# Optimization experiments

Measured on AMD Instinct MI355X. Metric: run time of the kernel, lower is better.

Reference implementation:

```python
import jax, jax.numpy as jnp
import numpy as np

N_ATOMS = 100000
M_NBR = 12
ORIG_FEA = 92
NBR_FEA = 41
AF = 64          # atom_fea_len
N_CONV = 3
OUT_DIM = 128
N_CRYSTALS = 2000
ATOMS_PER = 50
EPS = 1e-5


def setup_inputs() -> dict:
    key = jax.random.key(0)
    ks = jax.random.split(key, 12)
    inp = {
        "atom_fea": jax.random.normal(ks[0], (N_ATOMS, ORIG_FEA), dtype=jnp.float32),
        "nbr_fea": jax.random.normal(ks[1], (N_ATOMS, M_NBR, NBR_FEA), dtype=jnp.float32),
        "nbr_fea_idx": jax.random.randint(ks[2], (N_ATOMS, M_NBR), 0, N_ATOMS, dtype=jnp.int32),
        "crystal_atom_idx": jnp.arange(N_CRYSTALS * ATOMS_PER, dtype=jnp.int32).reshape(N_CRYSTALS, ATOMS_PER),
    }
    # parameters
    inp["W_embed"] = jax.random.normal(ks[3], (ORIG_FEA, AF), dtype=jnp.float32) * 0.05
    inp["b_embed"] = jnp.zeros((AF,), dtype=jnp.float32)
    in_full = 2 * AF + NBR_FEA  # 169
    inp["W_full"] = jax.random.normal(ks[4], (N_CONV, in_full, 2 * AF), dtype=jnp.float32) * 0.05
    inp["b_full"] = jnp.zeros((N_CONV, 2 * AF), dtype=jnp.float32)
    inp["bn1_gamma"] = jnp.ones((N_CONV, 2 * AF), dtype=jnp.float32)
    inp["bn1_beta"] = jnp.zeros((N_CONV, 2 * AF), dtype=jnp.float32)
    inp["bn2_gamma"] = jnp.ones((N_CONV, AF), dtype=jnp.float32)
    inp["bn2_beta"] = jnp.zeros((N_CONV, AF), dtype=jnp.float32)
    inp["W_pool"] = jax.random.normal(ks[5], (AF, OUT_DIM), dtype=jnp.float32) * 0.05
    inp["b_pool"] = jnp.zeros((OUT_DIM,), dtype=jnp.float32)
    return inp


def _batchnorm(x, gamma, beta):
    # training-mode BatchNorm1d over leading dim, biased variance
    m = jnp.mean(x, axis=0)
    v = jnp.var(x, axis=0)
    return (x - m) * jax.lax.rsqrt(v + EPS) * gamma + beta


def _conv_layer(x, nbr_fea, nbr_fea_idx, Wf, bf, g1, be1, g2, be2):
    N, M = nbr_fea_idx.shape
    nbr_atom = x[nbr_fea_idx]                                  # [N, M, AF] gather
    self_fea = jnp.broadcast_to(x[:, None, :], (N, M, AF))     # [N, M, AF]
    total = jnp.concatenate([self_fea, nbr_atom, nbr_fea], axis=2)  # [N, M, 2AF+NBR]
    gated = jnp.einsum('nmi,io->nmo', total, Wf) + bf          # [N, M, 2AF]
    gated = _batchnorm(gated.reshape(N * M, 2 * AF), g1, be1).reshape(N, M, 2 * AF)
    nbr_filter = jax.nn.sigmoid(gated[..., :AF])
    nbr_core = jax.nn.softplus(gated[..., AF:])
    nbr_sumed = jnp.sum(nbr_filter * nbr_core, axis=1)         # [N, AF]
    nbr_sumed = _batchnorm(nbr_sumed, g2, be2)
    return jax.nn.softplus(x + nbr_sumed)


def reference(atom_fea, nbr_fea, nbr_fea_idx, crystal_atom_idx,
              W_embed, b_embed, W_full, b_full,
              bn1_gamma, bn1_beta, bn2_gamma, bn2_beta,
              W_pool, b_pool):
    x = atom_fea @ W_embed + b_embed                           # [N, AF]
    for i in range(N_CONV):
        x = _conv_layer(x, nbr_fea, nbr_fea_idx,
                        W_full[i], b_full[i],
                        bn1_gamma[i], bn1_beta[i],
                        bn2_gamma[i], bn2_beta[i])
    crystal_fea = jnp.mean(x[crystal_atom_idx], axis=1)        # [G, AF] per-graph mean pool
    return jax.nn.relu(crystal_fea @ W_pool + b_pool)          # [G, OUT_DIM]
```

## Files before the change

### kernel.cpp

```cpp
#include <hip/hip_runtime.h>
#include <hip/hip_fp16.h>
#include <math.h>

#define N_ATOMS 100000
#define M_NBR 12
#define ORIG_FEA 92
#define NBR_FEA 41
#define AF 64
#define OUT2 128
#define IN_FULL 169
#define N_CONV 3
#define OUT_DIM 128
#define N_CRYSTALS 2000
#define ATOMS_PER 50
#define EPS 1e-5f

#define ZCH 16
#define EDGES (ZCH * M_NBR)
#define NF_STRIDE 44
#define YB_ATOMS 80
#define YB_CHUNK 16
#define ZP_BLOCKS 1024
#define NCHUNKS (N_ATOMS / ZCH)

typedef _Float16 h4 __attribute__((ext_vector_type(4)));

__device__ __forceinline__ float softplus_f(float x) {
    return fmaxf(x, 0.0f) + __logf(1.0f + __expf(-fabsf(x)));
}
__device__ __forceinline__ float sigmoid_f(float x) {
    return __builtin_amdgcn_rcpf(1.0f + __expf(-x));
}
__device__ __forceinline__ void fma4(float4& a, float s, const float4& b) {
    a.x = fmaf(s, b.x, a.x); a.y = fmaf(s, b.y, a.y);
    a.z = fmaf(s, b.z, a.z); a.w = fmaf(s, b.w, a.w);
}
__device__ __forceinline__ float4 zero4() { return make_float4(0.f, 0.f, 0.f, 0.f); }

union H4 { uint2 u; __half2 h[2]; };
__device__ __forceinline__ void store_h4(__half* p, float4 v) {
    H4 t;
    t.h[0] = __floats2half2_rn(v.x, v.y);
    t.h[1] = __floats2half2_rn(v.z, v.w);
    *(uint2*)p = t.u;
}
__device__ __forceinline__ float4 load_h4(const __half* p) {
    H4 t; t.u = *(const uint2*)p;
    float2 a = __half22float2(t.h[0]);
    float2 b = __half22float2(t.h[1]);
    return make_float4(a.x, a.y, b.x, b.y);
}

__global__ __launch_bounds__(256, 2) void k_embed(
    const float* __restrict__ af, const float* __restrict__ W,
    const float* __restrict__ b, float* __restrict__ x) {
  __shared__ __align__(16) float saf[64 * ORIG_FEA];
  int a0 = blockIdx.x * 64;
  int na = min(64, N_ATOMS - a0);
  int tid = threadIdx.x;
  int c = tid & 63, rgrp = tid >> 6;
  float w[ORIG_FEA];
#pragma unroll
  for (int k = 0; k < ORIG_FEA; ++k) w[k] = W[k * AF + c];
  int n4 = na * (ORIG_FEA / 4);
  const float4* g4 = (const float4*)(af + (size_t)a0 * ORIG_FEA);
  float4* s4 = (float4*)saf;
  for (int e = tid; e < n4; e += 256) s4[e] = g4[e];
  __syncthreads();
  float bc = b[c];
  for (int a = rgrp; a < na; a += 4) {
    float acc = bc;
    const float4* row = (const float4*)(saf + a * ORIG_FEA);
#pragma unroll
    for (int q = 0; q < ORIG_FEA / 4; ++q) {
      float4 v = row[q];
      acc = fmaf(v.x, w[4 * q], acc);
      acc = fmaf(v.y, w[4 * q + 1], acc);
      acc = fmaf(v.z, w[4 * q + 2], acc);
      acc = fmaf(v.w, w[4 * q + 3], acc);
    }
    x[(size_t)(a0 + a) * AF + c] = acc;
  }
}

__global__ __launch_bounds__(256, 2) void k_ysn(
    const float* __restrict__ x, const float* __restrict__ Wf,
    float* __restrict__ y_self, float* __restrict__ y_nbr) {
  __shared__ __align__(16) float sW2[64 * 256];
  __shared__ __align__(16) float sx[YB_CHUNK * AF];
  int tid = threadIdx.x;
  int cg = tid & 31, ag = tid >> 5;
  int c0 = cg * 4;
  {
    float4* s4 = (float4*)sW2;
    const float4* g4 = (const float4*)Wf;
    for (int e = tid; e < 64 * 64; e += 256) {
      int r = e >> 6, q = e & 63;
      s4[r * 64 + q] = (q < 32) ? g4[r * 32 + q] : g4[(64 + r) * 32 + (q - 32)];
    }
  }
  int ab = blockIdx.x * YB_ATOMS;
  for (int cc = 0; cc < YB_ATOMS / YB_CHUNK; ++cc) {
    int a0 = ab + cc * YB_CHUNK;
    __syncthreads();
    {
      float4* s4 = (float4*)sx;
      const float4* g4 = (const float4*)(x + (size_t)a0 * AF);
      for (int e = tid; e < YB_CHUNK * AF / 4; e += 256) s4[e] = g4[e];
    }
    __syncthreads();
    float4 accs[2] = {zero4(), zero4()};
    float4 accn[2] = {zero4(), zero4()};
    for (int k0 = 0; k0 < AF; k0 += 4) {
      float4 av0 = *(const float4*)(sx + (ag * 2 + 0) * AF + k0);
      float4 av1 = *(const float4*)(sx + (ag * 2 + 1) * AF + k0);
#pragma unroll
      for (int kk = 0; kk < 4; ++kk) {
        float4 b0 = *(const float4*)(sW2 + (k0 + kk) * 256 + c0);
        float4 b1 = *(const float4*)(sW2 + (k0 + kk) * 256 + 128 + c0);
        float s0 = (kk == 0) ? av0.x : (kk == 1) ? av0.y : (kk == 2) ? av0.z : av0.w;
        float s1 = (kk == 0) ? av1.x : (kk == 1) ? av1.y : (kk == 2) ? av1.z : av1.w;
        fma4(accs[0], s0, b0); fma4(accn[0], s0, b1);
        fma4(accs[1], s1, b0); fma4(accn[1], s1, b1);
      }
    }
#pragma unroll
    for (int t = 0; t < 2; ++t) {
      size_t n = (size_t)(a0 + ag * 2 + t);
      *(float4*)(y_self + n * OUT2 + c0) = accs[t];
      *(float4*)(y_nbr + n * OUT2 + c0) = accn[t];
    }
  }
}

__device__ __forceinline__ void edge_gemm(
    const _Float16* snf, const float* sW, int ebase, int c0,
    float4 acc0[6], float4 acc1[6]) {
#pragma unroll
  for (int e = 0; e < 6; ++e) { acc0[e] = zero4(); acc1[e] = zero4(); }
  for (int k0 = 0; k0 < 40; k0 += 4) {
    h4 av[6];
#pragma unroll
    for (int e = 0; e < 6; ++e)
      av[e] = *(const h4*)(snf + (ebase + e) * NF_STRIDE + k0);
#pragma unroll
    for (int kk = 0; kk < 4; ++kk) {
      float4 b0 = *(const float4*)(sW + (k0 + kk) * OUT2 + c0);
      float4 b1 = *(const float4*)(sW + (k0 + kk) * OUT2 + AF + c0);
#pragma unroll
      for (int e = 0; e < 6; ++e) {
        float s = (float)av[e][kk];
        fma4(acc0[e], s, b0);
        fma4(acc1[e], s, b1);
      }
    }
  }
  {
    float4 b0 = *(const float4*)(sW + 40 * OUT2 + c0);
    float4 b1 = *(const float4*)(sW + 40 * OUT2 + AF + c0);
#pragma unroll
    for (int e = 0; e < 6; ++e) {
      float s = (float)snf[(ebase + e) * NF_STRIDE + 40];
      fma4(acc0[e], s, b0);
      fma4(acc1[e], s, b1);
    }
  }
}

template <int WZ>
__global__ __launch_bounds__(256, 2) void k_zstats_p(
    const float* __restrict__ nbr_fea, const int* __restrict__ nidx,
    const float* __restrict__ y_self, const float* __restrict__ y_nbr,
    const float* __restrict__ Wf, const float* __restrict__ bf,
    float* __restrict__ gsum, float* __restrict__ gsumsq,
    __half* __restrict__ z16) {
  __shared__ __align__(16) _Float16 snf[2 * EDGES * NF_STRIDE];
  __shared__ __align__(16) float sW[NBR_FEA * OUT2];
  __shared__ __align__(16) unsigned char sbuf[1536];
  int tid = threadIdx.x;
  int cg = tid & 15, eg = tid >> 4;
  int c0 = cg * 4;
  {
    float4* sW4 = (float4*)sW;
    const float4* gW4 = (const float4*)(Wf + 2 * AF * OUT2);
    for (int e = tid; e < NBR_FEA * (OUT2 / 4); e += 256) sW4[e] = gW4[e];
  }
  {
    int a0 = blockIdx.x * ZCH;
    const float* gnf = nbr_fea + (size_t)a0 * M_NBR * NBR_FEA;
    _Float16* s = snf;
    int* si = (int*)sbuf;
    for (int e = tid; e < EDGES * NBR_FEA; e += 256) {
      int r = e / NBR_FEA;
      int k = e - r * NBR_FEA;
      s[r * NF_STRIDE + k] = (_Float16)gnf[e];
    }
    for (int e = tid; e < EDGES; e += 256) {
      s[e * NF_STRIDE + 41] = (_Float16)0.f;
      s[e * NF_STRIDE + 42] = (_Float16)0.f;
      s[e * NF_STRIDE + 43] = (_Float16)0.f;
      si[e] = nidx[(size_t)a0 * M_NBR + e];
    }
  }
  __syncthreads();
  float4 bz0 = *(const float4*)(bf + c0);
  float4 bz1 = *(const float4*)(bf + AF + c0);
  float4 sm0 = zero4(), sq0 = zero4(), sm1 = zero4(), sq1 = zero4();
  int buf = 0;
  for (int cc = blockIdx.x; cc < NCHUNKS; cc += ZP_BLOCKS) {
    int ccn = cc + ZP_BLOCKS;
    if (ccn < NCHUNKS) {
      int an = ccn * ZCH;
      const float* gnf = nbr_fea + (size_t)an * M_NBR * NBR_FEA;
      _Float16* s = snf + (buf ^ 1) * (EDGES * NF_STRIDE);
      int* si = (int*)sbuf + (buf ^ 1) * EDGES;
      for (int e = tid; e < EDGES * NBR_FEA; e += 256) {
        int r = e / NBR_FEA;
        int k = e - r * NBR_FEA;
        s[r * NF_STRIDE + k] = (_Float16)gnf[e];
      }
      for (int e = tid; e < EDGES; e += 256) {
        s[e * NF_STRIDE + 41] = (_Float16)0.f;
        s[e * NF_STRIDE + 42] = (_Float16)0.f;
        s[e * NF_STRIDE + 43] = (_Float16)0.f;
        si[e] = nidx[(size_t)an * M_NBR + e];
      }
    }
    int a0 = cc * ZCH;
    const _Float16* scur = snf + buf * (EDGES * NF_STRIDE);
    const int* sicur = (const int*)sbuf + buf * EDGES;
    for (int c = 0; c < 2; ++c) {
      int ebase = c * 96 + eg * 6;
      int atomL = c * 8 + (eg >> 1);
      const float* ys = y_self + (size_t)(a0 + atomL) * OUT2;
      float4 y0 = *(const float4*)(ys + c0);
      float4 y1 = *(const float4*)(ys + AF + c0);
      float4 acc0[6], acc1[6];
      edge_gemm(scur, sW, ebase, c0, acc0, acc1);
#pragma unroll
      for (int e = 0; e < 6; ++e) {
        int j = sicur[ebase + e];
        const float* yn = y_nbr + (size_t)j * OUT2;
        float4 n0 = *(const float4*)(yn + c0);
        float4 n1 = *(const float4*)(yn + AF + c0);
        float4 z0, z1;
        z0.x = acc0[e].x + y0.x + n0.x + bz0.x; z0.y = acc0[e].y + y0.y + n0.y + bz0.y;
        z0.z = acc0[e].z + y0.z + n0.z + bz0.z; z0.w = acc0[e].w + y0.w + n0.w + bz0.w;
        z1.x = acc1[e].x + y1.x + n1.x + bz1.x; z1.y = acc1[e].y + y1.y + n1.y + bz1.y;
        z1.z = acc1[e].z + y1.z + n1.z + bz1.z; z1.w = acc1[e].w + y1.w + n1.w + bz1.w;
        if (WZ) {
          __half* zp = z16 + ((size_t)a0 * M_NBR + ebase + e) * OUT2 + c0;
          store_h4(zp, z0);
          store_h4(zp + AF, z1);
        }
        sm0.x += z0.x; sm0.y += z0.y; sm0.z += z0.z; sm0.w += z0.w;
        sm1.x += z1.x; sm1.y += z1.y; sm1.z += z1.z; sm1.w += z1.w;
        sq0.x = fmaf(z0.x, z0.x, sq0.x); sq0.y = fmaf(z0.y, z0.y, sq0.y);
        sq0.z = fmaf(z0.z, z0.z, sq0.z); sq0.w = fmaf(z0.w, z0.w, sq0.w);
        sq1.x = fmaf(z1.x, z1.x, sq1.x); sq1.y = fmaf(z1.y, z1.y, sq1.y);
        sq1.z = fmaf(z1.z, z1.z, sq1.z); sq1.w = fmaf(z1.w, z1.w, sq1.w);
      }
    }
    __syncthreads();
    buf ^= 1;
  }
  float* lsum = (float*)sbuf;
  float* lsumsq = lsum + OUT2;
  ((float*)sbuf)[tid] = 0.f;
  __syncthreads();
  atomicAdd(&lsum[c0 + 0], sm0.x); atomicAdd(&lsum[c0 + 1], sm0.y);
  atomicAdd(&lsum[c0 + 2], sm0.z); atomicAdd(&lsum[c0 + 3], sm0.w);
  atomicAdd(&lsum[AF + c0 + 0], sm1.x); atomicAdd(&lsum[AF + c0 + 1], sm1.y);
  atomicAdd(&lsum[AF + c0 + 2], sm1.z); atomicAdd(&lsum[AF + c0 + 3], sm1.w);
  atomicAdd(&lsumsq[c0 + 0], sq0.x); atomicAdd(&lsumsq[c0 + 1], sq0.y);
  atomicAdd(&lsumsq[c0 + 2], sq0.z); atomicAdd(&lsumsq[c0 + 3], sq0.w);
  atomicAdd(&lsumsq[AF + c0 + 0], sq1.x); atomicAdd(&lsumsq[AF + c0 + 1], sq1.y);
  atomicAdd(&lsumsq[AF + c0 + 2], sq1.z); atomicAdd(&lsumsq[AF + c0 + 3], sq1.w);
  __syncthreads();
  if (tid < OUT2) {
    atomicAdd(&gsum[tid], lsum[tid]);
    atomicAdd(&gsumsq[tid], lsumsq[tid]);
  }
}

__device__ __forceinline__ void stage_edge(
    const float* __restrict__ nbr_fea, const int* __restrict__ nidx,
    const float* __restrict__ We, int a0, int tid,
    _Float16* snf, float* sW, int* sidx) {
  float4* sW4 = (float4*)sW;
  const float4* gW4 = (const float4*)We;
  for (int e = tid; e < NBR_FEA * (OUT2 / 4); e += 256) sW4[e] = gW4[e];
  const float* gnf = nbr_fea + (size_t)a0 * M_NBR * NBR_FEA;
  for (int e = tid; e < EDGES * NBR_FEA; e += 256) {
    int r = e / NBR_FEA;
    int k = e - r * NBR_FEA;
    snf[r * NF_STRIDE + k] = (_Float16)gnf[e];
  }
  for (int e = tid; e < EDGES; e += 256) {
    snf[e * NF_STRIDE + 41] = (_Float16)0.f;
    snf[e * NF_STRIDE + 42] = (_Float16)0.f;
    snf[e * NF_STRIDE + 43] = (_Float16)0.f;
    sidx[e] = nidx[(size_t)a0 * M_NBR + e];
  }
}

__global__ __launch_bounds__(256, 2) void k_zstats_fb(
    const float* __restrict__ nbr_fea, const int* __restrict__ nidx,
    const float* __restrict__ y_self, const float* __restrict__ y_nbr,
    const float* __restrict__ Wf, const float* __restrict__ bf,
    float* __restrict__ gsum, float* __restrict__ gsumsq) {
  __shared__ __align__(16) _Float16 snf[EDGES * NF_STRIDE];
  __shared__ __align__(16) float sW[NBR_FEA * OUT2];
  __shared__ int sidx[EDGES];
  __shared__ float lsum[OUT2], lsumsq[OUT2];
  int tid = threadIdx.x;
  int cg = tid & 15, eg = tid >> 4;
  int c0 = cg * 4;
  if (tid < OUT2) { lsum[tid] = 0.f; lsumsq[tid] = 0.f; }
  int a0 = blockIdx.x * ZCH;
  stage_edge(nbr_fea, nidx, Wf + 2 * AF * OUT2, a0, tid, snf, sW, sidx);
  __syncthreads();
  float4 bz0 = *(const float4*)(bf + c0);
  float4 bz1 = *(const float4*)(bf + AF + c0);
  float4 sm0 = zero4(), sq0 = zero4(), sm1 = zero4(), sq1 = zero4();
  for (int c = 0; c < 2; ++c) {
    int ebase = c * 96 + eg * 6;
    int atomL = c * 8 + (eg >> 1);
    const float* ys = y_self + (size_t)(a0 + atomL) * OUT2;
    float4 y0 = *(const float4*)(ys + c0);
    float4 y1 = *(const float4*)(ys + AF + c0);
    float4 acc0[6], acc1[6];
    edge_gemm(snf, sW, ebase, c0, acc0, acc1);
#pragma unroll
    for (int e = 0; e < 6; ++e) {
      int j = sidx[ebase + e];
      const float* yn = y_nbr + (size_t)j * OUT2;
      float4 n0 = *(const float4*)(yn + c0);
      float4 n1 = *(const float4*)(yn + AF + c0);
      float4 z0, z1;
      z0.x = acc0[e].x + y0.x + n0.x + bz0.x; z0.y = acc0[e].y + y0.y + n0.y + bz0.y;
      z0.z = acc0[e].z + y0.z + n0.z + bz0.z; z0.w = acc0[e].w + y0.w + n0.w + bz0.w;
      z1.x = acc1[e].x + y1.x + n1.x + bz1.x; z1.y = acc1[e].y + y1.y + n1.y + bz1.y;
      z1.z = acc1[e].z + y1.z + n1.z + bz1.z; z1.w = acc1[e].w + y1.w + n1.w + bz1.w;
      sm0.x += z0.x; sm0.y += z0.y; sm0.z += z0.z; sm0.w += z0.w;
      sm1.x += z1.x; sm1.y += z1.y; sm1.z += z1.z; sm1.w += z1.w;
      sq0.x = fmaf(z0.x, z0.x, sq0.x); sq0.y = fmaf(z0.y, z0.y, sq0.y);
      sq0.z = fmaf(z0.z, z0.z, sq0.z); sq0.w = fmaf(z0.w, z0.w, sq0.w);
      sq1.x = fmaf(z1.x, z1.x, sq1.x); sq1.y = fmaf(z1.y, z1.y, sq1.y);
      sq1.z = fmaf(z1.z, z1.z, sq1.z); sq1.w = fmaf(z1.w, z1.w, sq1.w);
    }
  }
  atomicAdd(&lsum[c0 + 0], sm0.x); atomicAdd(&lsum[c0 + 1], sm0.y);
  atomicAdd(&lsum[c0 + 2], sm0.z); atomicAdd(&lsum[c0 + 3], sm0.w);
  atomicAdd(&lsum[AF + c0 + 0], sm1.x); atomicAdd(&lsum[AF + c0 + 1], sm1.y);
  atomicAdd(&lsum[AF + c0 + 2], sm1.z); atomicAdd(&lsum[AF + c0 + 3], sm1.w);
  atomicAdd(&lsumsq[c0 + 0], sq0.x); atomicAdd(&lsumsq[c0 + 1], sq0.y);
  atomicAdd(&lsumsq[c0 + 2], sq0.z); atomicAdd(&lsumsq[c0 + 3], sq0.w);
  atomicAdd(&lsumsq[AF + c0 + 0], sq1.x); atomicAdd(&lsumsq[AF + c0 + 1], sq1.y);
  atomicAdd(&lsumsq[AF + c0 + 2], sq1.z); atomicAdd(&lsumsq[AF + c0 + 3], sq1.w);
  __syncthreads();
  if (tid < OUT2) {
    atomicAdd(&gsum[tid], lsum[tid]);
    atomicAdd(&gsumsq[tid], lsumsq[tid]);
  }
}

__global__ __launch_bounds__(256, 4) void k_apply_stream(
    const __half* __restrict__ z16,
    const float* __restrict__ sc1, const float* __restrict__ sh1,
    float* __restrict__ s_out, float* __restrict__ gsum, float* __restrict__ gsumsq) {
  __shared__ float lsum[AF], lsumsq[AF];
  int tid = threadIdx.x;
  if (tid < AF) { lsum[tid] = 0.f; lsumsq[tid] = 0.f; }
  __syncthreads();
  int cg = tid & 15, a = tid >> 4;
  int c0 = cg * 4;
  size_t atom = (size_t)blockIdx.x * 16 + a;
  float4 f0 = *(const float4*)(sc1 + c0);
  float4 g0 = *(const float4*)(sh1 + c0);
  float4 f1 = *(const float4*)(sc1 + AF + c0);
  float4 g1 = *(const float4*)(sh1 + AF + c0);
  const __half* zr = z16 + atom * (M_NBR * OUT2);
  float4 sacc = zero4();
#pragma unroll 4
  for (int m = 0; m < M_NBR; ++m) {
    float4 zf = load_h4(zr + m * OUT2 + c0);
    float4 zc = load_h4(zr + m * OUT2 + AF + c0);
    zf.x = fmaf(zf.x, f0.x, g0.x); zf.y = fmaf(zf.y, f0.y, g0.y);
    zf.z = fmaf(zf.z, f0.z, g0.z); zf.w = fmaf(zf.w, f0.w, g0.w);
    zc.x = fmaf(zc.x, f1.x, g1.x); zc.y = fmaf(zc.y, f1.y, g1.y);
    zc.z = fmaf(zc.z, f1.z, g1.z); zc.w = fmaf(zc.w, f1.w, g1.w);
    sacc.x = fmaf(sigmoid_f(zf.x), softplus_f(zc.x), sacc.x);
    sacc.y = fmaf(sigmoid_f(zf.y), softplus_f(zc.y), sacc.y);
    sacc.z = fmaf(sigmoid_f(zf.z), softplus_f(zc.z), sacc.z);
    sacc.w = fmaf(sigmoid_f(zf.w), softplus_f(zc.w), sacc.w);
  }
  *(float4*)(s_out + atom * AF + c0) = sacc;
  float4 sq;
  sq.x = sacc.x * sacc.x; sq.y = sacc.y * sacc.y;
  sq.z = sacc.z * sacc.z; sq.w = sacc.w * sacc.w;
  sacc.x += __shfl_xor(sacc.x, 16, 64); sacc.y += __shfl_xor(sacc.y, 16, 64);
  sacc.z += __shfl_xor(sacc.z, 16, 64); sacc.w += __shfl_xor(sacc.w, 16, 64);
  sq.x += __shfl_xor(sq.x, 16, 64); sq.y += __shfl_xor(sq.y, 16, 64);
  sq.z += __shfl_xor(sq.z, 16, 64); sq.w += __shfl_xor(sq.w, 16, 64);
  sacc.x += __shfl_xor(sacc.x, 32, 64); sacc.y += __shfl_xor(sacc.y, 32, 64);
  sacc.z += __shfl_xor(sacc.z, 32, 64); sacc.w += __shfl_xor(sacc.w, 32, 64);
  sq.x += __shfl_xor(sq.x, 32, 64); sq.y += __shfl_xor(sq.y, 32, 64);
  sq.z += __shfl_xor(sq.z, 32, 64); sq.w += __shfl_xor(sq.w, 32, 64);
  if ((tid & 48) == 0) {
    atomicAdd(&lsum[c0 + 0], sacc.x); atomicAdd(&lsum[c0 + 1], sacc.y);
    atomicAdd(&lsum[c0 + 2], sacc.z); atomicAdd(&lsum[c0 + 3], sacc.w);
    atomicAdd(&lsumsq[c0 + 0], sq.x); atomicAdd(&lsumsq[c0 + 1], sq.y);
    atomicAdd(&lsumsq[c0 + 2], sq.z); atomicAdd(&lsumsq[c0 + 3], sq.w);
  }
  __syncthreads();
  if (tid < AF) {
    atomicAdd(&gsum[tid], lsum[tid]);
    atomicAdd(&gsumsq[tid], lsumsq[tid]);
  }
}

__global__ __launch_bounds__(256, 2) void k_apply(
    const float* __restrict__ nbr_fea, const int* __restrict__ nidx,
    const float* __restrict__ y_self, const float* __restrict__ y_nbr,
    const float* __restrict__ Wf, const float* __restrict__ bf,
    const float* __restrict__ sc1, const float* __restrict__ sh1,
    float* __restrict__ s_out, float* __restrict__ gsum, float* __restrict__ gsumsq) {
  __shared__ __align__(16) _Float16 snf[EDGES * NF_STRIDE];
  __shared__ __align__(16) float sW[NBR_FEA * OUT2];
  __shared__ int sidx[EDGES];
  __shared__ float lsum[AF], lsumsq[AF];
  int tid = threadIdx.x;
  int cg = tid & 15, eg = tid >> 4;
  int c0 = cg * 4;
  if (tid < AF) { lsum[tid] = 0.f; lsumsq[tid] = 0.f; }
  int a0 = blockIdx.x * ZCH;
  stage_edge(nbr_fea, nidx, Wf + 2 * AF * OUT2, a0, tid, snf, sW, sidx);
  __syncthreads();
  float4 bz0 = *(const float4*)(bf + c0);
  float4 bz1 = *(const float4*)(bf + AF + c0);
  float4 f0 = *(const float4*)(sc1 + c0);
  float4 g0 = *(const float4*)(sh1 + c0);
  float4 f1 = *(const float4*)(sc1 + AF + c0);
  float4 g1 = *(const float4*)(sh1 + AF + c0);
  for (int c = 0; c < 2; ++c) {
    int ebase = c * 96 + eg * 6;
    int atomL = c * 8 + (eg >> 1);
    const float* ys = y_self + (size_t)(a0 + atomL) * OUT2;
    float4 y0 = *(const float4*)(ys + c0);
    float4 y1 = *(const float4*)(ys + AF + c0);
    float4 acc0[6], acc1[6];
    edge_gemm(snf, sW, ebase, c0, acc0, acc1);
    float4 sacc = zero4();
#pragma unroll
    for (int e = 0; e < 6; ++e) {
      int j = sidx[ebase + e];
      const float* yn = y_nbr + (size_t)j * OUT2;
      float4 n0 = *(const float4*)(yn + c0);
      float4 n1 = *(const float4*)(yn + AF + c0);
      float4 z0, z1;
      z0.x = fmaf(acc0[e].x + y0.x + n0.x + bz0.x, f0.x, g0.x);
      z0.y = fmaf(acc0[e].y + y0.y + n0.y + bz0.y, f0.y, g0.y);
      z0.z = fmaf(acc0[e].z + y0.z + n0.z + bz0.z, f0.z, g0.z);
      z0.w = fmaf(acc0[e].w + y0.w + n0.w + bz0.w, f0.w, g0.w);
      z1.x = fmaf(acc1[e].x + y1.x + n1.x + bz1.x, f1.x, g1.x);
      z1.y = fmaf(acc1[e].y + y1.y + n1.y + bz1.y, f1.y, g1.y);
      z1.z = fmaf(acc1[e].z + y1.z + n1.z + bz1.z, f1.z, g1.z);
      z1.w = fmaf(acc1[e].w + y1.w + n1.w + bz1.w, f1.w, g1.w);
      sacc.x = fmaf(sigmoid_f(z0.x), softplus_f(z1.x), sacc.x);
      sacc.y = fmaf(sigmoid_f(z0.y), softplus_f(z1.y), sacc.y);
      sacc.z = fmaf(sigmoid_f(z0.z), softplus_f(z1.z), sacc.z);
      sacc.w = fmaf(sigmoid_f(z0.w), softplus_f(z1.w), sacc.w);
    }
    sacc.x += __shfl_xor(sacc.x, 16, 64);
    sacc.y += __shfl_xor(sacc.y, 16, 64);
    sacc.z += __shfl_xor(sacc.z, 16, 64);
    sacc.w += __shfl_xor(sacc.w, 16, 64);
    if ((eg & 1) == 0) {
      *(float4*)(s_out + (size_t)(a0 + atomL) * AF + c0) = sacc;
      atomicAdd(&lsum[c0 + 0], sacc.x); atomicAdd(&lsum[c0 + 1], sacc.y);
      atomicAdd(&lsum[c0 + 2], sacc.z); atomicAdd(&lsum[c0 + 3], sacc.w);
      atomicAdd(&lsumsq[c0 + 0], sacc.x * sacc.x);
      atomicAdd(&lsumsq[c0 + 1], sacc.y * sacc.y);
      atomicAdd(&lsumsq[c0 + 2], sacc.z * sacc.z);
      atomicAdd(&lsumsq[c0 + 3], sacc.w * sacc.w);
    }
  }
  __syncthreads();
  if (tid < AF) {
    atomicAdd(&gsum[tid], lsum[tid]);
    atomicAdd(&gsumsq[tid], lsumsq[tid]);
  }
}

__global__ void k_finalize(const float* __restrict__ gsum, const float* __restrict__ gsumsq,
                           const float* __restrict__ gamma, const float* __restrict__ beta,
                           float* __restrict__ scale, float* __restrict__ shift,
                           int chn, float invcount) {
  int c = threadIdx.x;
  if (c < chn) {
    float m = gsum[c] * invcount;
    float v = gsumsq[c] * invcount - m * m;
    float sc = gamma[c] * rsqrtf(v + EPS);
    scale[c] = sc;
    shift[c] = beta[c] - m * sc;
  }
}

__global__ __launch_bounds__(256) void k_update(
    float* __restrict__ x, const float* __restrict__ s,
    const float* __restrict__ sc2, const float* __restrict__ sh2) {
  int e = blockIdx.x * 256 + threadIdx.x;
  if (e < N_ATOMS * AF) {
    int c = e & (AF - 1);
    float v = x[e] + s[e] * sc2[c] + sh2[c];
    x[e] = softplus_f(v);
  }
}

__global__ __launch_bounds__(128) void k_pool(
    const float* __restrict__ x, const int* __restrict__ cidx,
    const float* __restrict__ Wp, const float* __restrict__ bp,
    float* __restrict__ out) {
  __shared__ float part[2][AF];
  __shared__ float mean[AF];
  int g = blockIdx.x, tid = threadIdx.x;
  int c = tid & 63, h = tid >> 6;
  float acc = 0.f;
  for (int a = h; a < ATOMS_PER; a += 2) {
    int idx = cidx[g * ATOMS_PER + a];
    acc += x[(size_t)idx * AF + c];
  }
  part[h][c] = acc;
  __syncthreads();
  if (tid < AF) mean[tid] = (part[0][tid] + part[1][tid]) * (1.0f / ATOMS_PER);
  __syncthreads();
  float o = bp[tid];
#pragma unroll
  for (int k = 0; k < AF; ++k) o += mean[k] * Wp[k * OUT_DIM + tid];
  out[(size_t)g * OUT_DIM + tid] = fmaxf(o, 0.f);
}

extern "C" void kernel_launch(void* const* d_in, const int* in_sizes, int n_in,
                              void* d_out, int out_size, void* d_ws, size_t ws_size,
                              hipStream_t stream) {
  const float* atom_fea = (const float*)d_in[0];
  const float* nbr_fea  = (const float*)d_in[1];
  const int*   nbr_idx  = (const int*)d_in[2];
  const int*   cidx     = (const int*)d_in[3];
  const float* W_embed  = (const float*)d_in[4];
  const float* b_embed  = (const float*)d_in[5];
  const float* W_full   = (const float*)d_in[6];
  const float* b_full   = (const float*)d_in[7];
  const float* bn1_g    = (const float*)d_in[8];
  const float* bn1_b    = (const float*)d_in[9];
  const float* bn2_g    = (const float*)d_in[10];
  const float* bn2_b    = (const float*)d_in[11];
  const float* W_pool   = (const float*)d_in[12];
  const float* b_pool   = (const float*)d_in[13];
  float* out = (float*)d_out;

  float* ws = (float*)d_ws;
  size_t off = 0;
  float* x      = ws + off; off += (size_t)N_ATOMS * AF;
  float* y_self = ws + off; off += (size_t)N_ATOMS * OUT2;
  float* y_nbr  = ws + off; off += (size_t)N_ATOMS * OUT2;
  float* s_buf  = ws + off; off += (size_t)N_ATOMS * AF;
  float* sums   = ws + off; off += (size_t)N_CONV * 384;
  float* affine = ws + off; off += (size_t)N_CONV * 384;

  size_t base_bytes = (off * sizeof(float) + 255) & ~(size_t)255;
  size_t z_bytes = (size_t)N_ATOMS * M_NBR * OUT2 * sizeof(__half);
  bool fast = ws_size >= base_bytes + z_bytes;
  __half* z16 = fast ? (__half*)((char*)d_ws + base_bytes) : nullptr;

  hipMemsetAsync(sums, 0, (size_t)N_CONV * 384 * sizeof(float), stream);

  k_embed<<<(N_ATOMS + 63) / 64, 256, 0, stream>>>(atom_fea, W_embed, b_embed, x);

  for (int i = 0; i < N_CONV; ++i) {
    const float* Wf = W_full + (size_t)i * IN_FULL * OUT2;
    const float* bf = b_full + (size_t)i * OUT2;
    float* sum1   = sums + (size_t)i * 384;
    float* sumsq1 = sum1 + OUT2;
    float* sum2   = sumsq1 + OUT2;
    float* sumsq2 = sum2 + AF;
    float* sc1 = affine + (size_t)i * 384;
    float* sh1 = sc1 + OUT2;
    float* sc2 = sh1 + OUT2;
    float* sh2 = sc2 + AF;

    k_ysn<<<N_ATOMS / YB_ATOMS, 256, 0, stream>>>(x, Wf, y_self, y_nbr);
    if (fast) {
      k_zstats_p<1><<<ZP_BLOCKS, 256, 0, stream>>>(
          nbr_fea, nbr_idx, y_self, y_nbr, Wf, bf, sum1, sumsq1, z16);
    } else {
      k_zstats_fb<<<N_ATOMS / ZCH, 256, 0, stream>>>(
          nbr_fea, nbr_idx, y_self, y_nbr, Wf, bf, sum1, sumsq1);
    }
    k_finalize<<<1, 128, 0, stream>>>(sum1, sumsq1, bn1_g + i * OUT2, bn1_b + i * OUT2,
                                      sc1, sh1, OUT2, 1.0f / ((float)N_ATOMS * M_NBR));
    if (fast) {
      k_apply_stream<<<N_ATOMS / 16, 256, 0, stream>>>(z16, sc1, sh1, s_buf,
                                                       sum2, sumsq2);
    } else {
      k_apply<<<N_ATOMS / ZCH, 256, 0, stream>>>(nbr_fea, nbr_idx, y_self, y_nbr,
                                                 Wf, bf, sc1, sh1, s_buf, sum2, sumsq2);
    }
    k_finalize<<<1, 128, 0, stream>>>(sum2, sumsq2, bn2_g + i * AF, bn2_b + i * AF,
                                      sc2, sh2, AF, 1.0f / (float)N_ATOMS);
    k_update<<<(N_ATOMS * AF + 255) / 256, 256, 0, stream>>>(x, s_buf, sc2, sh2);
  }

  k_pool<<<N_CRYSTALS, 128, 0, stream>>>(x, cidx, W_pool, b_pool, out);
}
```

Measured before the change: 1.872 ms.

## Fuse BN finalize and residual update into consumer kernels

Removes the separate k_finalize and k_update launches in the fast path. Each consumer block now recomputes the BatchNorm scale and shift from the global sums. The residual softplus update runs inside the next layer's k_ysn load, which writes x back, and inside the final k_pool. This cuts kernel launches and one full read/write pass over x and s per layer, at the cost of redundant per-block finalize math and a read of s in k_ysn.

```diff
diff --git a/kernel.cpp b/kernel.cpp
--- a/kernel.cpp
+++ b/kernel.cpp
@@ -83,14 +83,27 @@
   }
 }
 
+template <int UPD>
 __global__ __launch_bounds__(256, 2) void k_ysn(
-    const float* __restrict__ x, const float* __restrict__ Wf,
-    float* __restrict__ y_self, float* __restrict__ y_nbr) {
+    const float* __restrict__ x, const float* __restrict__ s,
+    const float* __restrict__ gsum2, const float* __restrict__ gsumsq2,
+    const float* __restrict__ bn2g, const float* __restrict__ bn2b,
+    const float* __restrict__ Wf,
+    float* __restrict__ y_self, float* __restrict__ y_nbr,
+    float* __restrict__ xout) {
   __shared__ __align__(16) float sW2[64 * 256];
   __shared__ __align__(16) float sx[YB_CHUNK * AF];
+  __shared__ __align__(16) float ssc[AF], ssh[AF];
   int tid = threadIdx.x;
   int cg = tid & 31, ag = tid >> 5;
   int c0 = cg * 4;
+  if (UPD && tid < AF) {
+    float m = gsum2[tid] * (1.0f / (float)N_ATOMS);
+    float v = gsumsq2[tid] * (1.0f / (float)N_ATOMS) - m * m;
+    float sc = bn2g[tid] * rsqrtf(v + EPS);
+    ssc[tid] = sc;
+    ssh[tid] = bn2b[tid] - m * sc;
+  }
   {
     float4* s4 = (float4*)sW2;
     const float4* g4 = (const float4*)Wf;
@@ -106,7 +119,19 @@
     {
       float4* s4 = (float4*)sx;
       const float4* g4 = (const float4*)(x + (size_t)a0 * AF);
-      for (int e = tid; e < YB_CHUNK * AF / 4; e += 256) s4[e] = g4[e];
+      for (int e = tid; e < YB_CHUNK * AF / 4; e += 256) {
+        float4 xv = g4[e];
+        if (UPD) {
+          float4 sv = ((const float4*)(s + (size_t)a0 * AF))[e];
+          int c4 = (e & 15) * 4;
+          xv.x = softplus_f(fmaf(sv.x, ssc[c4 + 0], xv.x) + ssh[c4 + 0]);
+          xv.y = softplus_f(fmaf(sv.y, ssc[c4 + 1], xv.y) + ssh[c4 + 1]);
+          xv.z = softplus_f(fmaf(sv.z, ssc[c4 + 2], xv.z) + ssh[c4 + 2]);
+          xv.w = softplus_f(fmaf(sv.w, ssc[c4 + 3], xv.w) + ssh[c4 + 3]);
+          ((float4*)(xout + (size_t)a0 * AF))[e] = xv;
+        }
+        s4[e] = xv;
+      }
     }
     __syncthreads();
     float4 accs[2] = {zero4(), zero4()};
@@ -367,19 +392,29 @@
 
 __global__ __launch_bounds__(256, 4) void k_apply_stream(
     const __half* __restrict__ z16,
-    const float* __restrict__ sc1, const float* __restrict__ sh1,
+    const float* __restrict__ gsum1, const float* __restrict__ gsumsq1,
+    const float* __restrict__ bn1g, const float* __restrict__ bn1b,
     float* __restrict__ s_out, float* __restrict__ gsum, float* __restrict__ gsumsq) {
+  __shared__ __align__(16) float ssc1[OUT2], ssh1[OUT2];
   __shared__ float lsum[AF], lsumsq[AF];
   int tid = threadIdx.x;
   if (tid < AF) { lsum[tid] = 0.f; lsumsq[tid] = 0.f; }
+  if (tid < OUT2) {
+    const float inv = 1.0f / ((float)N_ATOMS * M_NBR);
+    float m = gsum1[tid] * inv;
+    float v = gsumsq1[tid] * inv - m * m;
+    float sc = bn1g[tid] * rsqrtf(v + EPS);
+    ssc1[tid] = sc;
+    ssh1[tid] = bn1b[tid] - m * sc;
+  }
   __syncthreads();
   int cg = tid & 15, a = tid >> 4;
   int c0 = cg * 4;
   size_t atom = (size_t)blockIdx.x * 16 + a;
-  float4 f0 = *(const float4*)(sc1 + c0);
-  float4 g0 = *(const float4*)(sh1 + c0);
-  float4 f1 = *(const float4*)(sc1 + AF + c0);
-  float4 g1 = *(const float4*)(sh1 + AF + c0);
+  float4 f0 = *(const float4*)(ssc1 + c0);
+  float4 g0 = *(const float4*)(ssh1 + c0);
+  float4 f1 = *(const float4*)(ssc1 + AF + c0);
+  float4 g1 = *(const float4*)(ssh1 + AF + c0);
   const __half* zr = z16 + atom * (M_NBR * OUT2);
   float4 sacc = zero4();
 #pragma unroll 4
@@ -507,29 +542,33 @@
   }
 }
 
-__global__ __launch_bounds__(256) void k_update(
-    float* __restrict__ x, const float* __restrict__ s,
-    const float* __restrict__ sc2, const float* __restrict__ sh2) {
-  int e = blockIdx.x * 256 + threadIdx.x;
-  if (e < N_ATOMS * AF) {
-    int c = e & (AF - 1);
-    float v = x[e] + s[e] * sc2[c] + sh2[c];
-    x[e] = softplus_f(v);
-  }
-}
-
 __global__ __launch_bounds__(128) void k_pool(
-    const float* __restrict__ x, const int* __restrict__ cidx,
+    const float* __restrict__ x, const float* __restrict__ s,
+    const float* __restrict__ gsum2, const float* __restrict__ gsumsq2,
+    const float* __restrict__ bn2g, const float* __restrict__ bn2b,
+    const int* __restrict__ cidx,
     const float* __restrict__ Wp, const float* __restrict__ bp,
     float* __restrict__ out) {
+  __shared__ float ssc[AF], ssh[AF];
   __shared__ float part[2][AF];
   __shared__ float mean[AF];
   int g = blockIdx.x, tid = threadIdx.x;
+  if (tid < AF) {
+    float m = gsum2[tid] * (1.0f / (float)N_ATOMS);
+    float v = gsumsq2[tid] * (1.0f / (float)N_ATOMS) - m * m;
+    float sc = bn2g[tid] * rsqrtf(v + EPS);
+    ssc[tid] = sc;
+    ssh[tid] = bn2b[tid] - m * sc;
+  }
+  __syncthreads();
   int c = tid & 63, h = tid >> 6;
+  float scc = ssc[c], shc = ssh[c];
   float acc = 0.f;
   for (int a = h; a < ATOMS_PER; a += 2) {
     int idx = cidx[g * ATOMS_PER + a];
-    acc += x[(size_t)idx * AF + c];
+    float xv = x[(size_t)idx * AF + c];
+    float sv = s[(size_t)idx * AF + c];
+    acc += softplus_f(fmaf(sv, scc, xv) + shc);
   }
   part[h][c] = acc;
   __syncthreads();
@@ -587,30 +626,38 @@
     float* sumsq2 = sum2 + AF;
     float* sc1 = affine + (size_t)i * 384;
     float* sh1 = sc1 + OUT2;
-    float* sc2 = sh1 + OUT2;
-    float* sh2 = sc2 + AF;
-
-    k_ysn<<<N_ATOMS / YB_ATOMS, 256, 0, stream>>>(x, Wf, y_self, y_nbr);
+
+    if (i == 0) {
+      k_ysn<0><<<N_ATOMS / YB_ATOMS, 256, 0, stream>>>(
+          x, nullptr, nullptr, nullptr, nullptr, nullptr, Wf, y_self, y_nbr, nullptr);
+    } else {
+      float* psum2   = sums + (size_t)(i - 1) * 384 + 2 * OUT2;
+      float* psumsq2 = psum2 + AF;
+      k_ysn<1><<<N_ATOMS / YB_ATOMS, 256, 0, stream>>>(
+          x, s_buf, psum2, psumsq2, bn2_g + (i - 1) * AF, bn2_b + (i - 1) * AF,
+          Wf, y_self, y_nbr, x);
+    }
     if (fast) {
       k_zstats_p<1><<<ZP_BLOCKS, 256, 0, stream>>>(
           nbr_fea, nbr_idx, y_self, y_nbr, Wf, bf, sum1, sumsq1, z16);
+      k_apply_stream<<<N_ATOMS / 16, 256, 0, stream>>>(
+          z16, sum1, sumsq1, bn1_g + i * OUT2, bn1_b + i * OUT2,
+          s_buf, sum2, sumsq2);
     } else {
       k_zstats_fb<<<N_ATOMS / ZCH, 256, 0, stream>>>(
           nbr_fea, nbr_idx, y_self, y_nbr, Wf, bf, sum1, sumsq1);
-    }
-    k_finalize<<<1, 128, 0, stream>>>(sum1, sumsq1, bn1_g + i * OUT2, bn1_b + i * OUT2,
-                                      sc1, sh1, OUT2, 1.0f / ((float)N_ATOMS * M_NBR));
-    if (fast) {
-      k_apply_stream<<<N_ATOMS / 16, 256, 0, stream>>>(z16, sc1, sh1, s_buf,
-                                                       sum2, sumsq2);
-    } else {
+      k_finalize<<<1, 128, 0, stream>>>(sum1, sumsq1, bn1_g + i * OUT2, bn1_b + i * OUT2,
+                                        sc1, sh1, OUT2, 1.0f / ((float)N_ATOMS * M_NBR));
       k_apply<<<N_ATOMS / ZCH, 256, 0, stream>>>(nbr_fea, nbr_idx, y_self, y_nbr,
                                                  Wf, bf, sc1, sh1, s_buf, sum2, sumsq2);
     }
-    k_finalize<<<1, 128, 0, stream>>>(sum2, sumsq2, bn2_g + i * AF, bn2_b + i * AF,
-                                      sc2, sh2, AF, 1.0f / (float)N_ATOMS);
-    k_update<<<(N_ATOMS * AF + 255) / 256, 256, 0, stream>>>(x, s_buf, sc2, sh2);
-  }
-
-  k_pool<<<N_CRYSTALS, 128, 0, stream>>>(x, cidx, W_pool, b_pool, out);
-}
+  }
+
+  {
+    float* fsum2   = sums + (size_t)(N_CONV - 1) * 384 + 2 * OUT2;
+    float* fsumsq2 = fsum2 + AF;
+    k_pool<<<N_CRYSTALS, 128, 0, stream>>>(
+        x, s_buf, fsum2, fsumsq2, bn2_g + (N_CONV - 1) * AF, bn2_b + (N_CONV - 1) * AF,
+        cidx, W_pool, b_pool, out);
+  }
+}
```

After: 1.815 ms. -3.1%, faster.
